# Kernel tuning notes

Measured on AMD Instinct MI355X. Metric: run time of the kernel, lower is better.

Reference implementation:

```python
import jax, jax.numpy as jnp
import numpy as np

N_NODES = 50000
N_EDGES = 800000
D_IN = 256
D_OUT = 64
NEG_SLOPE = 0.2


def setup_inputs() -> dict:
    key = jax.random.key(0)
    k_x, k_src, k_dst, k_val, k_w = jax.random.split(key, 5)
    x = jax.random.normal(k_x, (N_NODES, D_IN), dtype=jnp.float32)
    edge_src = jax.random.randint(k_src, (N_EDGES,), 0, N_NODES, dtype=jnp.int32)
    edge_dst = jnp.sort(jax.random.randint(k_dst, (N_EDGES,), 0, N_NODES, dtype=jnp.int32))
    edge_val = jax.random.uniform(k_val, (N_EDGES,), dtype=jnp.float32)
    # xavier_uniform for Linear weight [out, in]; zeros for bias
    limit = float(np.sqrt(6.0 / (D_IN + D_OUT)))
    W = jax.random.uniform(k_w, (D_OUT, D_IN), dtype=jnp.float32, minval=-limit, maxval=limit)
    b = jnp.zeros((D_OUT,), dtype=jnp.float32)
    return {"x": x, "W": W, "b": b, "edge_src": edge_src, "edge_dst": edge_dst, "edge_val": edge_val}


def reference(x, W, b, edge_src, edge_dst, edge_val):
    # support = x @ W^T + b  -> [N, D_OUT]
    support = jnp.einsum("ni,oi->no", x, W) + b
    # sparse adj matmul: out[d] = sum_{edges e with dst=d} val[e] * support[src[e]]
    messages = edge_val[:, None] * support[edge_src]  # [E, D_OUT]
    agg = jax.ops.segment_sum(messages, edge_dst, num_segments=N_NODES)
    return jnp.where(agg >= 0, agg, NEG_SLOPE * agg)
```

## Files before the change

### kernel.cpp

```cpp
#include <hip/hip_runtime.h>

#define N_NODES 50000
#define N_EDGES 800000
#define D_IN 256
#define D_OUT 64
#define NEG_SLOPE 0.2f

#define GEMM_BLOCKS 782
#define PREP2_BLOCKS 3125
#define GRID1 (GEMM_BLOCKS + PREP2_BLOCKS)

typedef __attribute__((ext_vector_type(8))) short bf16x8;
typedef __attribute__((ext_vector_type(4))) float f32x4;
typedef __attribute__((ext_vector_type(4))) int   i32x4;

__device__ inline ushort f2bf(float f) {
  union { float f; unsigned u; } v; v.f = f;
  unsigned r = v.u + 0x7FFFu + ((v.u >> 16) & 1u);
  return (ushort)(r >> 16);
}
__device__ inline float bf2f(ushort h) {
  union { unsigned u; float f; } v; v.u = ((unsigned)h) << 16;
  return v.f;
}

#define XLOAD(dst, off)                                                  \
  asm volatile("global_load_dwordx4 %0, %1, off offset:" #off            \
               : "=v"(dst) : "v"(xp) : "memory")

__global__ __launch_bounds__(256, 4) void gemm_prep(
    const float* __restrict__ x, const float* __restrict__ W,
    const float* __restrict__ bias,
    const int* __restrict__ edge_dst, int* __restrict__ row_ptr,
    ushort* __restrict__ support) {
  const int tid  = threadIdx.x;
  const int bid  = blockIdx.x;

  if (bid >= GEMM_BLOCKS) {
    const int e = (bid - GEMM_BLOCKS) * 256 + tid;
    if (e < N_EDGES) {
      const int d = edge_dst[e];
      if (e == 0) {
        for (int n = 0; n <= d; ++n) row_ptr[n] = 0;
      } else {
        const int dp = edge_dst[e - 1];
        if (d != dp)
          for (int n = dp + 1; n <= d; ++n) row_ptr[n] = e;
      }
      if (e == N_EDGES - 1)
        for (int n = d + 1; n <= N_NODES; ++n) row_ptr[n] = N_EDGES;
    }
    return;
  }

  __shared__ ushort Wl[D_OUT * D_IN];
  const int wave = tid >> 6;
  const int lane = tid & 63;
  const int m0  = bid * 64 + wave * 16;
  const int r16 = lane & 15;
  const int kg  = lane >> 4;
  int arow = m0 + r16;
  if (arow >= N_NODES) arow = N_NODES - 1;
  const float* xp = x + (size_t)arow * D_IN + kg * 8;

  f32x4 xd[16];
  XLOAD(xd[0], 0);    XLOAD(xd[1], 16);
  XLOAD(xd[2], 128);  XLOAD(xd[3], 144);
  XLOAD(xd[4], 256);  XLOAD(xd[5], 272);
  XLOAD(xd[6], 384);  XLOAD(xd[7], 400);
  XLOAD(xd[8], 512);  XLOAD(xd[9], 528);
  XLOAD(xd[10], 640); XLOAD(xd[11], 656);
  XLOAD(xd[12], 768); XLOAD(xd[13], 784);
  XLOAD(xd[14], 896); XLOAD(xd[15], 912);

  for (int c = tid; c < (D_OUT * D_IN) / 8; c += 256) {
    const int row = c >> 5;
    const int cc  = c & 31;
    const f32x4 w0 = *reinterpret_cast<const f32x4*>(W + c * 8);
    const f32x4 w1 = *reinterpret_cast<const f32x4*>(W + c * 8 + 4);
    bf16x8 v;
    v[0] = (short)f2bf(w0[0]); v[1] = (short)f2bf(w0[1]);
    v[2] = (short)f2bf(w0[2]); v[3] = (short)f2bf(w0[3]);
    v[4] = (short)f2bf(w1[0]); v[5] = (short)f2bf(w1[1]);
    v[6] = (short)f2bf(w1[2]); v[7] = (short)f2bf(w1[3]);
    unsigned byte = row * 512 + cc * 16;
    byte ^= (row & 7) << 4;
    *reinterpret_cast<bf16x8*>(reinterpret_cast<char*>(Wl) + byte) = v;
  }
  __syncthreads();

  asm volatile("s_waitcnt vmcnt(0)" ::: "memory");
  __builtin_amdgcn_sched_barrier(0);

  f32x4 acc[4] = {f32x4{0.f,0.f,0.f,0.f}, f32x4{0.f,0.f,0.f,0.f},
                  f32x4{0.f,0.f,0.f,0.f}, f32x4{0.f,0.f,0.f,0.f}};
#pragma unroll
  for (int ks = 0; ks < 8; ++ks) {
    const f32x4 xa = xd[2 * ks];
    const f32x4 xb = xd[2 * ks + 1];
    bf16x8 a;
    a[0] = (short)f2bf(xa[0]); a[1] = (short)f2bf(xa[1]);
    a[2] = (short)f2bf(xa[2]); a[3] = (short)f2bf(xa[3]);
    a[4] = (short)f2bf(xb[0]); a[5] = (short)f2bf(xb[1]);
    a[6] = (short)f2bf(xb[2]); a[7] = (short)f2bf(xb[3]);
#pragma unroll
    for (int nb = 0; nb < 4; ++nb) {
      const int row = nb * 16 + r16;
      unsigned byte = row * 512 + kg * 16 + ks * 64;
      byte ^= (row & 7) << 4;
      const bf16x8 bfrag = *reinterpret_cast<const bf16x8*>(
          reinterpret_cast<const char*>(Wl) + byte);
      acc[nb] =
          __builtin_amdgcn_mfma_f32_16x16x32_bf16(a, bfrag, acc[nb], 0, 0, 0);
    }
  }
#pragma unroll
  for (int nb = 0; nb < 4; ++nb) {
    const int col = nb * 16 + r16;
    const float bv = bias[col];
#pragma unroll
    for (int i = 0; i < 4; ++i) {
      const int row = m0 + kg * 4 + i;
      if (row < N_NODES)
        support[(size_t)row * D_OUT + col] = f2bf(acc[nb][i] + bv);
    }
  }
}

__global__ __launch_bounds__(256, 8) void agg_kernel(
    const ushort* __restrict__ support, const int* __restrict__ edge_src,
    const float* __restrict__ edge_val, const int* __restrict__ row_ptr,
    float* __restrict__ out) {
  const int wid = (blockIdx.x * 256 + threadIdx.x) >> 6;
  const int lane = threadIdx.x & 63;
  if (wid >= N_NODES) return;
  const int lo = row_ptr[wid];
  const int hi = row_ptr[wid + 1];

  float a[8];
#pragma unroll
  for (int q = 0; q < 8; ++q) a[q] = 0.f;

  int e = lo;
  for (; e + 16 <= hi; e += 16) {
    i32x4 s4[4];
    f32x4 v4[4];
#pragma unroll
    for (int qb = 0; qb < 4; ++qb) {
      __builtin_memcpy(&s4[qb], edge_src + e + qb * 4, 16);
      __builtin_memcpy(&v4[qb], edge_val + e + qb * 4, 16);
    }
#pragma unroll
    for (int qb = 0; qb < 4; ++qb)
#pragma unroll
      for (int j = 0; j < 4; ++j)
        a[(qb * 4 + j) & 7] = fmaf(
            v4[qb][j],
            bf2f(support[(size_t)s4[qb][j] * D_OUT + lane]),
            a[(qb * 4 + j) & 7]);
  }
  for (; e + 4 <= hi; e += 4) {
    i32x4 s4;
    f32x4 v4;
    __builtin_memcpy(&s4, edge_src + e, 16);
    __builtin_memcpy(&v4, edge_val + e, 16);
#pragma unroll
    for (int j = 0; j < 4; ++j)
      a[j] = fmaf(v4[j], bf2f(support[(size_t)s4[j] * D_OUT + lane]), a[j]);
  }
  for (; e < hi; ++e)
    a[0] = fmaf(edge_val[e], bf2f(support[(size_t)edge_src[e] * D_OUT + lane]), a[0]);

  const float acc = ((a[0] + a[1]) + (a[2] + a[3])) + ((a[4] + a[5]) + (a[6] + a[7]));
  out[(size_t)wid * D_OUT + lane] = acc >= 0.f ? acc : NEG_SLOPE * acc;
}

extern "C" void kernel_launch(void* const* d_in, const int* in_sizes, int n_in,
                              void* d_out, int out_size, void* d_ws, size_t ws_size,
                              hipStream_t stream) {
  const float* x        = (const float*)d_in[0];
  const float* W        = (const float*)d_in[1];
  const float* b        = (const float*)d_in[2];
  const int*   edge_src = (const int*)d_in[3];
  const int*   edge_dst = (const int*)d_in[4];
  const float* edge_val = (const float*)d_in[5];
  float* out = (float*)d_out;

  ushort* support = (ushort*)d_ws;
  char* p = (char*)d_ws + (size_t)N_NODES * D_OUT * sizeof(ushort);
  int* row_ptr = (int*)p;

  hipLaunchKernelGGL(gemm_prep, dim3(GRID1), dim3(256), 0, stream,
                     x, W, b, edge_dst, row_ptr, support);
  hipLaunchKernelGGL(agg_kernel, dim3((N_NODES * 64 + 255) / 256), dim3(256),
                     0, stream, support, edge_src, edge_val, row_ptr, out);
}
```

Before: 50.40 us.

## Process two destination nodes per wavefront with interleaved edge loops

```diff
diff --git a/kernel.cpp b/kernel.cpp
--- a/kernel.cpp
+++ b/kernel.cpp
@@ -127,52 +127,65 @@
   }
 }
 
-__global__ __launch_bounds__(256, 8) void agg_kernel(
+__global__ __launch_bounds__(256, 6) void agg_kernel(
     const ushort* __restrict__ support, const int* __restrict__ edge_src,
     const float* __restrict__ edge_val, const int* __restrict__ row_ptr,
     float* __restrict__ out) {
-  const int wid = (blockIdx.x * 256 + threadIdx.x) >> 6;
+  const int wp = (blockIdx.x * 256 + threadIdx.x) >> 6;
   const int lane = threadIdx.x & 63;
-  if (wid >= N_NODES) return;
-  const int lo = row_ptr[wid];
-  const int hi = row_ptr[wid + 1];
-
-  float a[8];
-#pragma unroll
-  for (int q = 0; q < 8; ++q) a[q] = 0.f;
-
-  int e = lo;
-  for (; e + 16 <= hi; e += 16) {
-    i32x4 s4[4];
-    f32x4 v4[4];
-#pragma unroll
-    for (int qb = 0; qb < 4; ++qb) {
-      __builtin_memcpy(&s4[qb], edge_src + e + qb * 4, 16);
-      __builtin_memcpy(&v4[qb], edge_val + e + qb * 4, 16);
-    }
-#pragma unroll
-    for (int qb = 0; qb < 4; ++qb)
-#pragma unroll
-      for (int j = 0; j < 4; ++j)
-        a[(qb * 4 + j) & 7] = fmaf(
-            v4[qb][j],
-            bf2f(support[(size_t)s4[qb][j] * D_OUT + lane]),
-            a[(qb * 4 + j) & 7]);
-  }
-  for (; e + 4 <= hi; e += 4) {
-    i32x4 s4;
-    f32x4 v4;
-    __builtin_memcpy(&s4, edge_src + e, 16);
-    __builtin_memcpy(&v4, edge_val + e, 16);
-#pragma unroll
-    for (int j = 0; j < 4; ++j)
-      a[j] = fmaf(v4[j], bf2f(support[(size_t)s4[j] * D_OUT + lane]), a[j]);
-  }
-  for (; e < hi; ++e)
-    a[0] = fmaf(edge_val[e], bf2f(support[(size_t)edge_src[e] * D_OUT + lane]), a[0]);
-
-  const float acc = ((a[0] + a[1]) + (a[2] + a[3])) + ((a[4] + a[5]) + (a[6] + a[7]));
-  out[(size_t)wid * D_OUT + lane] = acc >= 0.f ? acc : NEG_SLOPE * acc;
+  if (wp >= N_NODES / 2) return;
+  const int nA = wp * 2;
+  const int loA = row_ptr[nA];
+  const int hiA = row_ptr[nA + 1];
+  const int hiB = row_ptr[nA + 2];
+
+  int eA = loA, eB = hiA;
+  float aA[4] = {0.f, 0.f, 0.f, 0.f};
+  float aB[4] = {0.f, 0.f, 0.f, 0.f};
+
+  while (eA + 4 <= hiA && eB + 4 <= hiB) {
+    i32x4 sA, sB;
+    f32x4 vA, vB;
+    __builtin_memcpy(&sA, edge_src + eA, 16);
+    __builtin_memcpy(&vA, edge_val + eA, 16);
+    __builtin_memcpy(&sB, edge_src + eB, 16);
+    __builtin_memcpy(&vB, edge_val + eB, 16);
+#pragma unroll
+    for (int j = 0; j < 4; ++j)
+      aA[j] = fmaf(vA[j], bf2f(support[(size_t)sA[j] * D_OUT + lane]), aA[j]);
+#pragma unroll
+    for (int j = 0; j < 4; ++j)
+      aB[j] = fmaf(vB[j], bf2f(support[(size_t)sB[j] * D_OUT + lane]), aB[j]);
+    eA += 4;
+    eB += 4;
+  }
+  for (; eA + 4 <= hiA; eA += 4) {
+    i32x4 s4; f32x4 v4;
+    __builtin_memcpy(&s4, edge_src + eA, 16);
+    __builtin_memcpy(&v4, edge_val + eA, 16);
+#pragma unroll
+    for (int j = 0; j < 4; ++j)
+      aA[j] = fmaf(v4[j], bf2f(support[(size_t)s4[j] * D_OUT + lane]), aA[j]);
+  }
+  for (; eA < hiA; ++eA)
+    aA[0] = fmaf(edge_val[eA],
+                 bf2f(support[(size_t)edge_src[eA] * D_OUT + lane]), aA[0]);
+  for (; eB + 4 <= hiB; eB += 4) {
+    i32x4 s4; f32x4 v4;
+    __builtin_memcpy(&s4, edge_src + eB, 16);
+    __builtin_memcpy(&v4, edge_val + eB, 16);
+#pragma unroll
+    for (int j = 0; j < 4; ++j)
+      aB[j] = fmaf(v4[j], bf2f(support[(size_t)s4[j] * D_OUT + lane]), aB[j]);
+  }
+  for (; eB < hiB; ++eB)
+    aB[0] = fmaf(edge_val[eB],
+                 bf2f(support[(size_t)edge_src[eB] * D_OUT + lane]), aB[0]);
+
+  const float rA = (aA[0] + aA[1]) + (aA[2] + aA[3]);
+  out[(size_t)nA * D_OUT + lane] = rA >= 0.f ? rA : NEG_SLOPE * rA;
+  const float rB = (aB[0] + aB[1]) + (aB[2] + aB[3]);
+  out[(size_t)(nA + 1) * D_OUT + lane] = rB >= 0.f ? rB : NEG_SLOPE * rB;
 }
 
 extern "C" void kernel_launch(void* const* d_in, const int* in_sizes, int n_in,
@@ -192,6 +205,7 @@
 
   hipLaunchKernelGGL(gemm_prep, dim3(GRID1), dim3(256), 0, stream,
                      x, W, b, edge_dst, row_ptr, support);
-  hipLaunchKernelGGL(agg_kernel, dim3((N_NODES * 64 + 255) / 256), dim3(256),
-                     0, stream, support, edge_src, edge_val, row_ptr, out);
-}
+  hipLaunchKernelGGL(agg_kernel, dim3((N_NODES / 2 * 64 + 255) / 256),
+                     dim3(256), 0, stream,
+                     support, edge_src, edge_val, row_ptr, out);
+}
```

Measured after the change: 49.18 us, median of 2. 2.4% less time.
